# Optimization experiments

Measured on AMD Instinct MI355X. Metric: run time of the kernel, lower is better.

The kernel has to match this reference:

```python
import jax, jax.numpy as jnp
import numpy as np

LAMBDA_1 = 1.0
LAMBDA_2 = 0.5


def setup_inputs() -> dict:
    key = jax.random.key(0)
    k1, k2, k3, k4, k5 = jax.random.split(key, 5)
    N_TRAIN, N_UNL, C = 4096, 32768, 1000
    G, K = 512, 64
    return {
        "train_logits": jax.random.normal(k1, (N_TRAIN, C), dtype=jnp.float32),
        "train_targets": jax.random.randint(k2, (N_TRAIN,), 0, C, dtype=jnp.int64),
        "unlabeled_logits": jax.random.normal(k3, (N_UNL, C), dtype=jnp.float32),
        "centroid_ids": jax.random.randint(k4, (G,), 0, N_TRAIN, dtype=jnp.int64),
        "member_ids": jax.random.randint(k5, (G, K), 0, N_UNL, dtype=jnp.int64),
    }


def reference(train_logits, train_targets, unlabeled_logits, centroid_ids, member_ids):
    N_unl = unlabeled_logits.shape[0]
    G, K = member_ids.shape

    # --- cross-entropy (mean) ---
    logp = jax.nn.log_softmax(train_logits, axis=-1)
    ce = -jnp.mean(jnp.take_along_axis(logp, train_targets[:, None], axis=1))

    # --- gather group tensors ---
    centroids = train_logits[centroid_ids]          # [G, C]
    members = unlabeled_logits[member_ids]          # [G, K, C]

    # --- alignment: sum_g sum_k ||centroid_g - member_gk||_2 / N_unl ---
    align = jnp.sum(jnp.linalg.norm(centroids[:, None, :] - members, axis=-1)) / N_unl

    # --- robustness: per-group upper-triangle pairwise L2 sums / (K * N_unl) ---
    sq = jnp.sum(members * members, axis=-1)                       # [G, K]
    gram = jnp.einsum("gkc,glc->gkl", members, members)            # [G, K, K]
    d2 = jnp.maximum(sq[:, :, None] + sq[:, None, :] - 2.0 * gram, 0.0)
    dist = jnp.sqrt(jnp.where(d2 > 0, d2, 1.0)) * (d2 > 0)         # safe sqrt
    iu = jnp.triu(jnp.ones((K, K), dtype=dist.dtype), k=1)         # i < j pairs
    robust = jnp.sum(dist * iu) / (K * N_unl)

    return ce + LAMBDA_1 * align + LAMBDA_2 * robust
```

## Files before the change

kernel.cpp:

```cpp
#include <hip/hip_runtime.h>

#define N_TRAIN 4096
#define N_UNL   32768
#define C_DIM   1000
#define G_GRP   512
#define K_MEM   64

#define CE_BLOCKS (N_TRAIN / 16)
#define NBLK      (G_GRP + CE_BLOCKS)

#define CHUNKS  8
#define CCOLS   128
#define PITCH_B 272
#define ROWS    80

typedef short        short8 __attribute__((ext_vector_type(8)));
typedef float        f32x4  __attribute__((ext_vector_type(4)));
typedef unsigned int u32x2  __attribute__((ext_vector_type(2)));
typedef unsigned int u32x4  __attribute__((ext_vector_type(4)));

__device__ __forceinline__ unsigned int pack_bf(float a, float b) {
    unsigned int ua = __float_as_uint(a) + 0x8000u;
    unsigned int ub = __float_as_uint(b) + 0x8000u;
    return (ua >> 16) | (ub & 0xffff0000u);
}

__global__ __launch_bounds__(256) void fused_kernel(const float* __restrict__ train,
                                                    const int*   __restrict__ targets,
                                                    const float* __restrict__ unl,
                                                    const int*   __restrict__ cids,
                                                    const int*   __restrict__ mids,
                                                    float* __restrict__ out) {
    __shared__ __align__(16) unsigned short bf[ROWS * (PITCH_B / 2)];
    __shared__ int   ids_sh[K_MEM];
    __shared__ float sq_sh[K_MEM];
    __shared__ float red_sh[256];
    __shared__ float sqc_sh;

    const int tid  = threadIdx.x;
    const int w    = tid >> 6;
    const int lane = tid & 63;

    if (blockIdx.x >= G_GRP) {
        const int blk = (int)blockIdx.x - G_GRP;
        float ce = 0.f;
        for (int r4 = 0; r4 < 4; ++r4) {
            const int row = blk * 16 + w * 4 + r4;
            const float* rp = train + (long)row * C_DIM;
            float x[16];
#pragma unroll
            for (int i = 0; i < 16; ++i) {
                int c = lane + i * 64;
                x[i] = (c < C_DIM) ? rp[c] : -1e30f;
            }
            float m = x[0];
#pragma unroll
            for (int i = 1; i < 16; ++i) m = fmaxf(m, x[i]);
#pragma unroll
            for (int off = 32; off > 0; off >>= 1) m = fmaxf(m, __shfl_xor(m, off, 64));
            float s = 0.f;
#pragma unroll
            for (int i = 0; i < 16; ++i) s += __expf(x[i] - m);
#pragma unroll
            for (int off = 32; off > 0; off >>= 1) s += __shfl_xor(s, off, 64);
            if (lane == 0) {
                int t = targets[row];
                ce += -(rp[t] - m - __logf(s));
            }
        }
        if (lane == 0) red_sh[w] = ce;
        __syncthreads();
        if (tid == 0)
            atomicAdd(out, (red_sh[0] + red_sh[1] + red_sh[2] + red_sh[3]) *
                           (1.0f / (float)N_TRAIN));
        return;
    }

    const int g    = blockIdx.x;
    const int quad = lane >> 4;
    const int c16  = lane & 15;

    if (tid < 255)
        *(u32x4*)((char*)bf + 65 * PITCH_B + tid * 16) = (u32x4){0, 0, 0, 0};
    if (tid < K_MEM) ids_sh[tid] = mids[g * K_MEM + tid];
    __syncthreads();

    const int rgrp = tid >> 5;
    const int l32  = tid & 31;
    const int cid  = cids[g];

    const float* srcb[8];
#pragma unroll
    for (int i = 0; i < 8; ++i)
        srcb[i] = unl + (long)ids_sh[rgrp + 8 * i] * C_DIM + l32 * 4;
    const float* csrc = train + (long)cid * C_DIM + l32 * 4;

    f32x4 acc[4], accC, accD;
#pragma unroll
    for (int t = 0; t < 4; ++t) acc[t] = (f32x4){0.f, 0.f, 0.f, 0.f};
    accC = (f32x4){0.f, 0.f, 0.f, 0.f};
    accD = (f32x4){0.f, 0.f, 0.f, 0.f};

    const float4 z4 = make_float4(0.f, 0.f, 0.f, 0.f);

    float4 mreg[8];
    float4 creg;

    {
        const bool v = (l32 * 4 < C_DIM);
#pragma unroll
        for (int i = 0; i < 8; ++i) mreg[i] = v ? *(const float4*)(srcb[i]) : z4;
        if (tid < 32) creg = *(const float4*)(csrc);
    }

    for (int ch = 0; ch < CHUNKS; ++ch) {
        __syncthreads();

#pragma unroll
        for (int i = 0; i < 8; ++i) {
            u32x2 h = {pack_bf(mreg[i].x, mreg[i].y), pack_bf(mreg[i].z, mreg[i].w)};
            *(u32x2*)((char*)bf + (rgrp + 8 * i) * PITCH_B + l32 * 8) = h;
        }
        if (tid < 32) {
            u32x2 h = {pack_bf(creg.x, creg.y), pack_bf(creg.z, creg.w)};
            *(u32x2*)((char*)bf + 64 * PITCH_B + tid * 8) = h;
        }
        __syncthreads();

        if (ch + 1 < CHUNKS) {
            const int col = (ch + 1) * CCOLS + l32 * 4;
            const bool v = (col < C_DIM);
            const long off = (long)(ch + 1) * CCOLS;
#pragma unroll
            for (int i = 0; i < 8; ++i) mreg[i] = v ? *(const float4*)(srcb[i] + off) : z4;
            if (tid < 32) creg = v ? *(const float4*)(csrc + off) : z4;
        }

#pragma unroll
        for (int s = 0; s < 4; ++s) {
            const int kbb = s * 64 + quad * 16;
            const char* base = (const char*)bf;
            short8 b0 = *(const short8*)(base + (0 * 16 + c16) * PITCH_B + kbb);
            short8 b1 = *(const short8*)(base + (1 * 16 + c16) * PITCH_B + kbb);
            short8 b2 = *(const short8*)(base + (2 * 16 + c16) * PITCH_B + kbb);
            short8 b3 = *(const short8*)(base + (3 * 16 + c16) * PITCH_B + kbb);
            short8 aM = *(const short8*)(base + (w * 16 + c16) * PITCH_B + kbb);
            short8 aC = *(const short8*)(base + (64 + c16) * PITCH_B + kbb);
            acc[0] = __builtin_amdgcn_mfma_f32_16x16x32_bf16(aM, b0, acc[0], 0, 0, 0);
            acc[1] = __builtin_amdgcn_mfma_f32_16x16x32_bf16(aM, b1, acc[1], 0, 0, 0);
            acc[2] = __builtin_amdgcn_mfma_f32_16x16x32_bf16(aM, b2, acc[2], 0, 0, 0);
            acc[3] = __builtin_amdgcn_mfma_f32_16x16x32_bf16(aM, b3, acc[3], 0, 0, 0);
            accC   = __builtin_amdgcn_mfma_f32_16x16x32_bf16(aC, aM, accC, 0, 0, 0);
            if (w == 0)
                accD = __builtin_amdgcn_mfma_f32_16x16x32_bf16(aC, aC, accD, 0, 0, 0);
        }
    }

#pragma unroll
    for (int t = 0; t < 4; ++t) {
        if (t == w) {
#pragma unroll
            for (int r = 0; r < 4; ++r)
                if (c16 == quad * 4 + r) sq_sh[w * 16 + c16] = acc[t][r];
        }
    }
    if (tid == 0) sqc_sh = accD[0];
    __syncthreads();

    float local = 0.f;
    if (quad == 0) {
        const int j = w * 16 + c16;
        const float d2 = sqc_sh + sq_sh[j] - 2.f * accC[0];
        if (d2 > 0.f) local += sqrtf(d2) * (1.0f / (float)N_UNL);
    }
#pragma unroll
    for (int t = 0; t < 4; ++t) {
#pragma unroll
        for (int r = 0; r < 4; ++r) {
            const int i = w * 16 + quad * 4 + r;
            const int j = t * 16 + c16;
            if (j > i) {
                const float d2 = sq_sh[i] + sq_sh[j] - 2.f * acc[t][r];
                if (d2 > 0.f)
                    local += sqrtf(d2) * (0.5f / ((float)K_MEM * (float)N_UNL));
            }
        }
    }

    red_sh[tid] = local;
    __syncthreads();
#pragma unroll
    for (int s = 128; s > 0; s >>= 1) {
        if (tid < s) red_sh[tid] += red_sh[tid + s];
        __syncthreads();
    }
    if (tid == 0) atomicAdd(out, red_sh[0]);
}

extern "C" void kernel_launch(void* const* d_in, const int* in_sizes, int n_in,
                              void* d_out, int out_size, void* d_ws, size_t ws_size,
                              hipStream_t stream) {
    (void)in_sizes; (void)n_in; (void)d_ws; (void)ws_size;
    const float* train_logits  = (const float*)d_in[0];
    const int*   train_targets = (const int*)d_in[1];
    const float* unl           = (const float*)d_in[2];
    const int*   centroid_ids  = (const int*)d_in[3];
    const int*   member_ids    = (const int*)d_in[4];
    float* out = (float*)d_out;

    hipMemsetAsync(out, 0, (size_t)out_size * sizeof(float), stream);
    fused_kernel<<<NBLK, 256, 0, stream>>>(train_logits, train_targets, unl,
                                           centroid_ids, member_ids, out);
}
```

Before: 210.2 us.

## Double-buffer LDS chunks with two-deep register prefetch and wave-shuffle reduction

Staging of member and centroid rows now alternates between two LDS buffers, so each chunk needs one barrier instead of two. Two register sets hold prefetched chunks, keeping global loads two chunks ahead of the MFMA work and putting more gather latency in flight. The MFMA section runs at raised wave priority, launch bounds request 3 blocks per CU, and the final 256-entry LDS tree reduction becomes wave shuffles plus a 4-entry sum. The cost is double the LDS footprint and more VGPRs, which could limit occupancy or cause spills.

```diff
diff --git a/kernel.cpp b/kernel.cpp
--- a/kernel.cpp
+++ b/kernel.cpp
@@ -25,16 +25,16 @@
     return (ua >> 16) | (ub & 0xffff0000u);
 }
 
-__global__ __launch_bounds__(256) void fused_kernel(const float* __restrict__ train,
-                                                    const int*   __restrict__ targets,
-                                                    const float* __restrict__ unl,
-                                                    const int*   __restrict__ cids,
-                                                    const int*   __restrict__ mids,
-                                                    float* __restrict__ out) {
-    __shared__ __align__(16) unsigned short bf[ROWS * (PITCH_B / 2)];
+__global__ __launch_bounds__(256, 3) void fused_kernel(const float* __restrict__ train,
+                                                       const int*   __restrict__ targets,
+                                                       const float* __restrict__ unl,
+                                                       const int*   __restrict__ cids,
+                                                       const int*   __restrict__ mids,
+                                                       float* __restrict__ out) {
+    __shared__ __align__(16) unsigned short bf[2][ROWS * (PITCH_B / 2)];
     __shared__ int   ids_sh[K_MEM];
     __shared__ float sq_sh[K_MEM];
-    __shared__ float red_sh[256];
+    __shared__ float red_sh[4];
     __shared__ float sqc_sh;
 
     const int tid  = threadIdx.x;
@@ -80,8 +80,10 @@
     const int quad = lane >> 4;
     const int c16  = lane & 15;
 
-    if (tid < 255)
-        *(u32x4*)((char*)bf + 65 * PITCH_B + tid * 16) = (u32x4){0, 0, 0, 0};
+    if (tid < 255) {
+        *(u32x4*)((char*)bf[0] + 65 * PITCH_B + tid * 16) = (u32x4){0, 0, 0, 0};
+        *(u32x4*)((char*)bf[1] + 65 * PITCH_B + tid * 16) = (u32x4){0, 0, 0, 0};
+    }
     if (tid < K_MEM) ids_sh[tid] = mids[g * K_MEM + tid];
     __syncthreads();
 
@@ -103,58 +105,65 @@
 
     const float4 z4 = make_float4(0.f, 0.f, 0.f, 0.f);
 
-    float4 mreg[8];
-    float4 creg;
-
-    {
-        const bool v = (l32 * 4 < C_DIM);
-#pragma unroll
-        for (int i = 0; i < 8; ++i) mreg[i] = v ? *(const float4*)(srcb[i]) : z4;
-        if (tid < 32) creg = *(const float4*)(csrc);
-    }
-
-    for (int ch = 0; ch < CHUNKS; ++ch) {
-        __syncthreads();
-
-#pragma unroll
-        for (int i = 0; i < 8; ++i) {
-            u32x2 h = {pack_bf(mreg[i].x, mreg[i].y), pack_bf(mreg[i].z, mreg[i].w)};
-            *(u32x2*)((char*)bf + (rgrp + 8 * i) * PITCH_B + l32 * 8) = h;
-        }
-        if (tid < 32) {
-            u32x2 h = {pack_bf(creg.x, creg.y), pack_bf(creg.z, creg.w)};
-            *(u32x2*)((char*)bf + 64 * PITCH_B + tid * 8) = h;
-        }
-        __syncthreads();
-
-        if (ch + 1 < CHUNKS) {
-            const int col = (ch + 1) * CCOLS + l32 * 4;
-            const bool v = (col < C_DIM);
-            const long off = (long)(ch + 1) * CCOLS;
-#pragma unroll
-            for (int i = 0; i < 8; ++i) mreg[i] = v ? *(const float4*)(srcb[i] + off) : z4;
-            if (tid < 32) creg = v ? *(const float4*)(csrc + off) : z4;
-        }
-
-#pragma unroll
-        for (int s = 0; s < 4; ++s) {
-            const int kbb = s * 64 + quad * 16;
-            const char* base = (const char*)bf;
-            short8 b0 = *(const short8*)(base + (0 * 16 + c16) * PITCH_B + kbb);
-            short8 b1 = *(const short8*)(base + (1 * 16 + c16) * PITCH_B + kbb);
-            short8 b2 = *(const short8*)(base + (2 * 16 + c16) * PITCH_B + kbb);
-            short8 b3 = *(const short8*)(base + (3 * 16 + c16) * PITCH_B + kbb);
-            short8 aM = *(const short8*)(base + (w * 16 + c16) * PITCH_B + kbb);
-            short8 aC = *(const short8*)(base + (64 + c16) * PITCH_B + kbb);
-            acc[0] = __builtin_amdgcn_mfma_f32_16x16x32_bf16(aM, b0, acc[0], 0, 0, 0);
-            acc[1] = __builtin_amdgcn_mfma_f32_16x16x32_bf16(aM, b1, acc[1], 0, 0, 0);
-            acc[2] = __builtin_amdgcn_mfma_f32_16x16x32_bf16(aM, b2, acc[2], 0, 0, 0);
-            acc[3] = __builtin_amdgcn_mfma_f32_16x16x32_bf16(aM, b3, acc[3], 0, 0, 0);
-            accC   = __builtin_amdgcn_mfma_f32_16x16x32_bf16(aC, aM, accC, 0, 0, 0);
-            if (w == 0)
-                accD = __builtin_amdgcn_mfma_f32_16x16x32_bf16(aC, aC, accD, 0, 0, 0);
-        }
-    }
+    float4 regA[8], regB[8];
+    float4 cregA, cregB;
+#pragma unroll
+    for (int i = 0; i < 8; ++i) regA[i] = *(const float4*)(srcb[i]);
+    if (tid < 32) cregA = *(const float4*)(csrc);
+#pragma unroll
+    for (int i = 0; i < 8; ++i) regB[i] = *(const float4*)(srcb[i] + CCOLS);
+    if (tid < 32) cregB = *(const float4*)(csrc + CCOLS);
+
+#define CHUNK_BODY(MR, CR, CH)                                                       \
+    do {                                                                             \
+        unsigned short* const bufp = bf[(CH) & 1];                                   \
+        _Pragma("unroll")                                                            \
+        for (int i = 0; i < 8; ++i) {                                                \
+            u32x2 h = {pack_bf(MR[i].x, MR[i].y), pack_bf(MR[i].z, MR[i].w)};        \
+            *(u32x2*)((char*)bufp + (rgrp + 8 * i) * PITCH_B + l32 * 8) = h;         \
+        }                                                                            \
+        if (tid < 32) {                                                              \
+            u32x2 h = {pack_bf(CR.x, CR.y), pack_bf(CR.z, CR.w)};                    \
+            *(u32x2*)((char*)bufp + 64 * PITCH_B + tid * 8) = h;                     \
+        }                                                                            \
+        if ((CH) + 2 < CHUNKS) {                                                     \
+            const int  col = ((CH) + 2) * CCOLS + l32 * 4;                           \
+            const bool v   = (col < C_DIM);                                          \
+            const long off = (long)(((CH) + 2) * CCOLS);                             \
+            _Pragma("unroll")                                                        \
+            for (int i = 0; i < 8; ++i)                                              \
+                MR[i] = v ? *(const float4*)(srcb[i] + off) : z4;                    \
+            if (tid < 32) CR = v ? *(const float4*)(csrc + off) : z4;                \
+        }                                                                            \
+        __syncthreads();                                                             \
+        __builtin_amdgcn_s_setprio(1);                                               \
+        _Pragma("unroll")                                                            \
+        for (int s = 0; s < 4; ++s) {                                                \
+            const int   kbb  = s * 64 + quad * 16;                                   \
+            const char* base = (const char*)bufp;                                    \
+            short8 b0 = *(const short8*)(base + (0 * 16 + c16) * PITCH_B + kbb);     \
+            short8 b1 = *(const short8*)(base + (1 * 16 + c16) * PITCH_B + kbb);     \
+            short8 b2 = *(const short8*)(base + (2 * 16 + c16) * PITCH_B + kbb);     \
+            short8 b3 = *(const short8*)(base + (3 * 16 + c16) * PITCH_B + kbb);     \
+            short8 aM = *(const short8*)(base + (w * 16 + c16) * PITCH_B + kbb);     \
+            short8 aC = *(const short8*)(base + (64 + c16) * PITCH_B + kbb);         \
+            acc[0] = __builtin_amdgcn_mfma_f32_16x16x32_bf16(aM, b0, acc[0], 0,0,0); \
+            acc[1] = __builtin_amdgcn_mfma_f32_16x16x32_bf16(aM, b1, acc[1], 0,0,0); \
+            acc[2] = __builtin_amdgcn_mfma_f32_16x16x32_bf16(aM, b2, acc[2], 0,0,0); \
+            acc[3] = __builtin_amdgcn_mfma_f32_16x16x32_bf16(aM, b3, acc[3], 0,0,0); \
+            accC   = __builtin_amdgcn_mfma_f32_16x16x32_bf16(aC, aM, accC, 0,0,0);   \
+            if (w == 0)                                                              \
+                accD = __builtin_amdgcn_mfma_f32_16x16x32_bf16(aC, aC, accD, 0,0,0); \
+        }                                                                            \
+        __builtin_amdgcn_s_setprio(0);                                               \
+    } while (0)
+
+#pragma unroll
+    for (int cc = 0; cc < CHUNKS; cc += 2) {
+        CHUNK_BODY(regA, cregA, cc);
+        CHUNK_BODY(regB, cregB, cc + 1);
+    }
+#undef CHUNK_BODY
 
 #pragma unroll
     for (int t = 0; t < 4; ++t) {
@@ -187,14 +196,11 @@
         }
     }
 
-    red_sh[tid] = local;
+#pragma unroll
+    for (int off = 32; off > 0; off >>= 1) local += __shfl_xor(local, off, 64);
+    if (lane == 0) red_sh[w] = local;
     __syncthreads();
-#pragma unroll
-    for (int s = 128; s > 0; s >>= 1) {
-        if (tid < s) red_sh[tid] += red_sh[tid + s];
-        __syncthreads();
-    }
-    if (tid == 0) atomicAdd(out, red_sh[0]);
+    if (tid == 0) atomicAdd(out, red_sh[0] + red_sh[1] + red_sh[2] + red_sh[3]);
 }
 
 extern "C" void kernel_launch(void* const* d_in, const int* in_sizes, int n_in,
```

Result: faster. 204.4 us (-2.8%).

## Double-buffer LDS tiles with per-wave row loads and a single barrier per chunk

Applied to the files above, without the earlier changes.

Restructures the group path so each wave loads its own 16 member rows as 256-column float4 slabs. Each slab feeds two 128-column chunks written into alternating LDS buffers, which leaves one barrier per chunk instead of two. The centroid dot product now uses a broadcast centroid row as the B operand, which drops the padded zero rows. The change also vectorises the cross-entropy loads, adds an occupancy hint and MFMA priority raising, and replaces the shared-memory tree reduction with wave shuffles. The aim is more memory-level parallelism and less synchronisation in a latency-bound gather, at the cost of higher register pressure from holding 16 float4 per thread.

```diff
diff --git a/kernel.cpp b/kernel.cpp
--- a/kernel.cpp
+++ b/kernel.cpp
@@ -12,12 +12,11 @@
 #define CHUNKS  8
 #define CCOLS   128
 #define PITCH_B 272
-#define ROWS    80
+#define ROWS    65
 
 typedef short        short8 __attribute__((ext_vector_type(8)));
 typedef float        f32x4  __attribute__((ext_vector_type(4)));
 typedef unsigned int u32x2  __attribute__((ext_vector_type(2)));
-typedef unsigned int u32x4  __attribute__((ext_vector_type(4)));
 
 __device__ __forceinline__ unsigned int pack_bf(float a, float b) {
     unsigned int ua = __float_as_uint(a) + 0x8000u;
@@ -25,16 +24,21 @@
     return (ua >> 16) | (ub & 0xffff0000u);
 }
 
-__global__ __launch_bounds__(256) void fused_kernel(const float* __restrict__ train,
-                                                    const int*   __restrict__ targets,
-                                                    const float* __restrict__ unl,
-                                                    const int*   __restrict__ cids,
-                                                    const int*   __restrict__ mids,
-                                                    float* __restrict__ out) {
-    __shared__ __align__(16) unsigned short bf[ROWS * (PITCH_B / 2)];
+__device__ __forceinline__ void lds_barrier() {
+    asm volatile("s_waitcnt lgkmcnt(0)" ::: "memory");
+    __builtin_amdgcn_s_barrier();
+}
+
+__global__ __launch_bounds__(256, 3) void fused_kernel(const float* __restrict__ train,
+                                                       const int*   __restrict__ targets,
+                                                       const float* __restrict__ unl,
+                                                       const int*   __restrict__ cids,
+                                                       const int*   __restrict__ mids,
+                                                       float* __restrict__ out) {
+    __shared__ __align__(16) unsigned short bf[2][ROWS * (PITCH_B / 2)];
     __shared__ int   ids_sh[K_MEM];
     __shared__ float sq_sh[K_MEM];
-    __shared__ float red_sh[256];
+    __shared__ float red_sh[4];
     __shared__ float sqc_sh;
 
     const int tid  = threadIdx.x;
@@ -47,20 +51,24 @@
         for (int r4 = 0; r4 < 4; ++r4) {
             const int row = blk * 16 + w * 4 + r4;
             const float* rp = train + (long)row * C_DIM;
-            float x[16];
-#pragma unroll
-            for (int i = 0; i < 16; ++i) {
-                int c = lane + i * 64;
-                x[i] = (c < C_DIM) ? rp[c] : -1e30f;
-            }
-            float m = x[0];
-#pragma unroll
-            for (int i = 1; i < 16; ++i) m = fmaxf(m, x[i]);
+            float4 x[4];
+#pragma unroll
+            for (int i = 0; i < 4; ++i) {
+                const int cb = lane * 4 + i * 256;
+                x[i] = (cb < C_DIM) ? *(const float4*)(rp + cb)
+                                    : make_float4(-1e30f, -1e30f, -1e30f, -1e30f);
+            }
+            float m = fmaxf(fmaxf(x[0].x, x[0].y), fmaxf(x[0].z, x[0].w));
+#pragma unroll
+            for (int i = 1; i < 4; ++i)
+                m = fmaxf(m, fmaxf(fmaxf(x[i].x, x[i].y), fmaxf(x[i].z, x[i].w)));
 #pragma unroll
             for (int off = 32; off > 0; off >>= 1) m = fmaxf(m, __shfl_xor(m, off, 64));
             float s = 0.f;
 #pragma unroll
-            for (int i = 0; i < 16; ++i) s += __expf(x[i] - m);
+            for (int i = 0; i < 4; ++i)
+                s += __expf(x[i].x - m) + __expf(x[i].y - m) +
+                     __expf(x[i].z - m) + __expf(x[i].w - m);
 #pragma unroll
             for (int off = 32; off > 0; off >>= 1) s += __shfl_xor(s, off, 64);
             if (lane == 0) {
@@ -80,20 +88,16 @@
     const int quad = lane >> 4;
     const int c16  = lane & 15;
 
-    if (tid < 255)
-        *(u32x4*)((char*)bf + 65 * PITCH_B + tid * 16) = (u32x4){0, 0, 0, 0};
     if (tid < K_MEM) ids_sh[tid] = mids[g * K_MEM + tid];
     __syncthreads();
 
-    const int rgrp = tid >> 5;
-    const int l32  = tid & 31;
-    const int cid  = cids[g];
-
-    const float* srcb[8];
-#pragma unroll
-    for (int i = 0; i < 8; ++i)
-        srcb[i] = unl + (long)ids_sh[rgrp + 8 * i] * C_DIM + l32 * 4;
-    const float* csrc = train + (long)cid * C_DIM + l32 * 4;
+    unsigned int roff[16];
+#pragma unroll
+    for (int i = 0; i < 16; ++i)
+        roff[i] = (unsigned int)ids_sh[w * 16 + i] * (unsigned int)(C_DIM * 4);
+    const unsigned int coff = (unsigned int)cids[g] * (unsigned int)(C_DIM * 4);
+    const char* const ubase = (const char*)unl;
+    const char* const tbase = (const char*)train;
 
     f32x4 acc[4], accC, accD;
 #pragma unroll
@@ -103,57 +107,63 @@
 
     const float4 z4 = make_float4(0.f, 0.f, 0.f, 0.f);
 
-    float4 mreg[8];
+    float4 regs[16];
     float4 creg;
 
     {
-        const bool v = (l32 * 4 < C_DIM);
-#pragma unroll
-        for (int i = 0; i < 8; ++i) mreg[i] = v ? *(const float4*)(srcb[i]) : z4;
-        if (tid < 32) creg = *(const float4*)(csrc);
-    }
-
+        const long ob = (long)lane * 16;
+#pragma unroll
+        for (int i = 0; i < 16; ++i)
+            regs[i] = *(const float4*)(ubase + roff[i] + ob);
+        if (w == 3) creg = *(const float4*)(tbase + coff + ob);
+    }
+
+#pragma unroll
     for (int ch = 0; ch < CHUNKS; ++ch) {
-        __syncthreads();
-
-#pragma unroll
-        for (int i = 0; i < 8; ++i) {
-            u32x2 h = {pack_bf(mreg[i].x, mreg[i].y), pack_bf(mreg[i].z, mreg[i].w)};
-            *(u32x2*)((char*)bf + (rgrp + 8 * i) * PITCH_B + l32 * 8) = h;
-        }
-        if (tid < 32) {
-            u32x2 h = {pack_bf(creg.x, creg.y), pack_bf(creg.z, creg.w)};
-            *(u32x2*)((char*)bf + 64 * PITCH_B + tid * 8) = h;
-        }
-        __syncthreads();
-
-        if (ch + 1 < CHUNKS) {
-            const int col = (ch + 1) * CCOLS + l32 * 4;
-            const bool v = (col < C_DIM);
-            const long off = (long)(ch + 1) * CCOLS;
-#pragma unroll
-            for (int i = 0; i < 8; ++i) mreg[i] = v ? *(const float4*)(srcb[i] + off) : z4;
-            if (tid < 32) creg = v ? *(const float4*)(csrc + off) : z4;
-        }
-
+        unsigned short* const bufp = bf[ch & 1];
+        const int l32 = lane & 31;
+        if ((ch & 1) == 0 ? (lane < 32) : (lane >= 32)) {
+#pragma unroll
+            for (int i = 0; i < 16; ++i) {
+                u32x2 h = {pack_bf(regs[i].x, regs[i].y), pack_bf(regs[i].z, regs[i].w)};
+                *(u32x2*)((char*)bufp + (w * 16 + i) * PITCH_B + l32 * 8) = h;
+            }
+            if (w == 3) {
+                u32x2 h = {pack_bf(creg.x, creg.y), pack_bf(creg.z, creg.w)};
+                *(u32x2*)((char*)bufp + 64 * PITCH_B + l32 * 8) = h;
+            }
+        }
+        if ((ch & 1) == 1 && ch + 1 < CHUNKS) {
+            const int  sc = (ch + 1) >> 1;
+            const int  cb = sc * 256 + lane * 4;
+            const bool v  = (cb < C_DIM);
+            const long ob = (long)cb * 4;
+#pragma unroll
+            for (int i = 0; i < 16; ++i)
+                regs[i] = v ? *(const float4*)(ubase + roff[i] + ob) : z4;
+            if (w == 3) creg = v ? *(const float4*)(tbase + coff + ob) : z4;
+        }
+        lds_barrier();
+        __builtin_amdgcn_s_setprio(1);
 #pragma unroll
         for (int s = 0; s < 4; ++s) {
-            const int kbb = s * 64 + quad * 16;
-            const char* base = (const char*)bf;
+            const int   kbb  = s * 64 + quad * 16;
+            const char* base = (const char*)bufp;
             short8 b0 = *(const short8*)(base + (0 * 16 + c16) * PITCH_B + kbb);
             short8 b1 = *(const short8*)(base + (1 * 16 + c16) * PITCH_B + kbb);
             short8 b2 = *(const short8*)(base + (2 * 16 + c16) * PITCH_B + kbb);
             short8 b3 = *(const short8*)(base + (3 * 16 + c16) * PITCH_B + kbb);
             short8 aM = *(const short8*)(base + (w * 16 + c16) * PITCH_B + kbb);
-            short8 aC = *(const short8*)(base + (64 + c16) * PITCH_B + kbb);
+            short8 bC = *(const short8*)(base + 64 * PITCH_B + kbb);
             acc[0] = __builtin_amdgcn_mfma_f32_16x16x32_bf16(aM, b0, acc[0], 0, 0, 0);
             acc[1] = __builtin_amdgcn_mfma_f32_16x16x32_bf16(aM, b1, acc[1], 0, 0, 0);
             acc[2] = __builtin_amdgcn_mfma_f32_16x16x32_bf16(aM, b2, acc[2], 0, 0, 0);
             acc[3] = __builtin_amdgcn_mfma_f32_16x16x32_bf16(aM, b3, acc[3], 0, 0, 0);
-            accC   = __builtin_amdgcn_mfma_f32_16x16x32_bf16(aC, aM, accC, 0, 0, 0);
+            accC = __builtin_amdgcn_mfma_f32_16x16x32_bf16(aM, bC, accC, 0, 0, 0);
             if (w == 0)
-                accD = __builtin_amdgcn_mfma_f32_16x16x32_bf16(aC, aC, accD, 0, 0, 0);
-        }
+                accD = __builtin_amdgcn_mfma_f32_16x16x32_bf16(bC, bC, accD, 0, 0, 0);
+        }
+        __builtin_amdgcn_s_setprio(0);
     }
 
 #pragma unroll
@@ -168,10 +178,13 @@
     __syncthreads();
 
     float local = 0.f;
-    if (quad == 0) {
-        const int j = w * 16 + c16;
-        const float d2 = sqc_sh + sq_sh[j] - 2.f * accC[0];
-        if (d2 > 0.f) local += sqrtf(d2) * (1.0f / (float)N_UNL);
+    if (c16 == 0) {
+#pragma unroll
+        for (int r = 0; r < 4; ++r) {
+            const int j = w * 16 + quad * 4 + r;
+            const float d2 = sqc_sh + sq_sh[j] - 2.f * accC[r];
+            if (d2 > 0.f) local += sqrtf(d2) * (1.0f / (float)N_UNL);
+        }
     }
 #pragma unroll
     for (int t = 0; t < 4; ++t) {
@@ -187,14 +200,11 @@
         }
     }
 
-    red_sh[tid] = local;
+#pragma unroll
+    for (int off = 32; off > 0; off >>= 1) local += __shfl_xor(local, off, 64);
+    if (lane == 0) red_sh[w] = local;
     __syncthreads();
-#pragma unroll
-    for (int s = 128; s > 0; s >>= 1) {
-        if (tid < s) red_sh[tid] += red_sh[tid + s];
-        __syncthreads();
-    }
-    if (tid == 0) atomicAdd(out, red_sh[0]);
+    if (tid == 0) atomicAdd(out, red_sh[0] + red_sh[1] + red_sh[2] + red_sh[3]);
 }
 
 extern "C" void kernel_launch(void* const* d_in, const int* in_sizes, int n_in,
```

Result: no change. 207.9 us (-1.1%).
